# Optimization experiments

Hardware: AMD Instinct MI355X
Metric: run time of the kernel (lower is better)

Reference implementation:

```python
import jax, jax.numpy as jnp
import numpy as np

N, E, F_IN, HD, H, G, NG, OUT = 50000, 800000, 128, 64, 4, 512, 50, 64
HC = HD * H  # 256
LN_EPS = 1e-5

def _lin(k, fi, fo):
    return jax.random.normal(k, (fi, fo), jnp.float32) / np.sqrt(fi).astype(np.float32)

def setup_inputs() -> dict:
    key = jax.random.key(0)
    ks = jax.random.split(key, 26)
    x = jax.random.normal(ks[0], (N, F_IN), jnp.float32)
    edge_index = jax.random.randint(ks[1], (2, E), 0, N)
    batch = jnp.sort(jax.random.randint(ks[2], (N,), 0, G))
    group_ids = jax.random.randint(ks[3], (N,), 0, NG)
    inp = {
        'x': x, 'edge_index': edge_index, 'batch': batch, 'group_ids': group_ids,
        'group_table': jax.random.normal(ks[4], (NG, HD), jnp.float32),
        'inW': _lin(ks[5], F_IN + HD, HD), 'inb': jnp.zeros((HD,), jnp.float32),
        'inln_g': jnp.ones((HD,), jnp.float32), 'inln_b': jnp.zeros((HD,), jnp.float32),
        'W0': _lin(ks[6], HD, HC), 'as0': jax.random.normal(ks[7], (H, HD), jnp.float32) * 0.1,
        'ad0': jax.random.normal(ks[8], (H, HD), jnp.float32) * 0.1, 'b0': jnp.zeros((HC,), jnp.float32),
        'ln0g': jnp.ones((HC,), jnp.float32), 'ln0b': jnp.zeros((HC,), jnp.float32),
        'W1': _lin(ks[9], HC, HC), 'as1': jax.random.normal(ks[10], (H, HD), jnp.float32) * 0.1,
        'ad1': jax.random.normal(ks[11], (H, HD), jnp.float32) * 0.1, 'b1': jnp.zeros((HC,), jnp.float32),
        'ln1g': jnp.ones((HC,), jnp.float32), 'ln1b': jnp.zeros((HC,), jnp.float32),
        'fc1W': _lin(ks[12], HC, HD), 'fc1b': jnp.zeros((HD,), jnp.float32),
        'fc2W': _lin(ks[13], HD, OUT), 'fc2b': jnp.zeros((OUT,), jnp.float32),
    }
    return inp

def _layer_norm(x, g, b):
    mu = jnp.mean(x, axis=-1, keepdims=True)
    var = jnp.mean(jnp.square(x - mu), axis=-1, keepdims=True)
    return (x - mu) * jax.lax.rsqrt(var + LN_EPS) * g + b

def _gat_conv(x, src, dst, W, a_src, a_dst, bias):
    # x: [N, Fin] -> per-head projection [N, H, HD]
    xl = (x @ W).reshape(-1, H, HD)
    al_s = jnp.einsum('nhc,hc->nh', xl, a_src)  # [N, H]
    al_d = jnp.einsum('nhc,hc->nh', xl, a_dst)
    e = jax.nn.leaky_relu(al_s[src] + al_d[dst], 0.2)  # [Etot, H]
    m = jax.ops.segment_max(e, dst, num_segments=N)    # stable softmax over in-edges
    ex = jnp.exp(e - m[dst])
    s = jax.ops.segment_sum(ex, dst, num_segments=N)
    alpha = ex / (s[dst] + 1e-16)
    msg = xl[src] * alpha[:, :, None]                   # [Etot, H, HD]
    out = jax.ops.segment_sum(msg, dst, num_segments=N)
    return out.reshape(-1, HC) + bias

def reference(x, edge_index, batch, group_ids, group_table, inW, inb, inln_g, inln_b,
              W0, as0, ad0, b0, ln0g, ln0b, W1, as1, ad1, b1, ln1g, ln1b,
              fc1W, fc1b, fc2W, fc2b):
    # group embedding concat + input projection (Linear -> LN -> GELU)
    h = jnp.concatenate([x, group_table[group_ids]], axis=-1)
    h = jax.nn.gelu(_layer_norm(h @ inW + inb, inln_g, inln_b), approximate=False)
    # add self-loops (PyG GATConv default)
    loop = jnp.arange(N)
    src = jnp.concatenate([edge_index[0], loop])
    dst = jnp.concatenate([edge_index[1], loop])
    # layer 0: dims 64 -> 256, no residual (width mismatch)
    h = jax.nn.gelu(_layer_norm(_gat_conv(h, src, dst, W0, as0, ad0, b0), ln0g, ln0b), approximate=False)
    # layer 1: 256 -> 256, residual applies
    identity = h
    h = jax.nn.gelu(_layer_norm(_gat_conv(h, src, dst, W1, as1, ad1, b1), ln1g, ln1b), approximate=False)
    h = h + identity
    # global mean pool over graphs
    sums = jax.ops.segment_sum(h, batch, num_segments=G)
    cnt = jax.ops.segment_sum(jnp.ones((N, 1), h.dtype), batch, num_segments=G)
    pooled = sums / jnp.maximum(cnt, 1.0)
    z = jax.nn.gelu(pooled @ fc1W + fc1b, approximate=False)
    logits = z @ fc2W + fc2b
    return jax.nn.log_softmax(logits, axis=1)
```

## Files before the change

kernel.cpp:

```cpp
#include <hip/hip_runtime.h>
#include <math.h>

#define N_NODES 50000
#define N_EDGES 800000
#define ETOT (N_EDGES + N_NODES)
#define F_IN 128
#define HD 64
#define NHEAD 4
#define HC 256
#define NGRAPH 512
#define NOUT 64
#define LN_EPS 1e-5f

typedef __attribute__((ext_vector_type(8))) short bf16x8;
typedef __attribute__((ext_vector_type(4))) float f32x4;
typedef __attribute__((ext_vector_type(2))) float f32x2;

__device__ __forceinline__ float wave_sum(float v) {
#pragma unroll
    for (int m = 1; m < 64; m <<= 1) v += __shfl_xor(v, m, 64);
    return v;
}
__device__ __forceinline__ float wave_max(float v) {
#pragma unroll
    for (int m = 1; m < 64; m <<= 1) v = fmaxf(v, __shfl_xor(v, m, 64));
    return v;
}
__device__ __forceinline__ float red16(float v) {
    v += __shfl_xor(v, 1, 64);
    v += __shfl_xor(v, 2, 64);
    v += __shfl_xor(v, 4, 64);
    v += __shfl_xor(v, 8, 64);
    return v;
}
__device__ __forceinline__ float gelu_exact(float x) {
    return 0.5f * x * (1.0f + erff(x * 0.70710678118654752f));
}
__device__ __forceinline__ unsigned short f2bf(float x) {
    unsigned int u = __float_as_uint(x);
    return (unsigned short)((u + 0x7fffu + ((u >> 16) & 1u)) >> 16);
}
__device__ __forceinline__ float bf2f(unsigned short u) {
    return __uint_as_float(((unsigned int)u) << 16);
}

__global__ void k_count(const int* __restrict__ ei, int* __restrict__ deg) {
    int t = blockIdx.x * blockDim.x + threadIdx.x;
    if (t >= ETOT) return;
    int dst = (t < N_EDGES) ? ei[N_EDGES + t] : (t - N_EDGES);
    atomicAdd(deg + dst, 1);
}

__global__ void k_scan(const int* __restrict__ deg, int* __restrict__ rowptr,
                       int* __restrict__ cursor) {
    __shared__ int wsum[16];
    __shared__ int chunk_total;
    int tid = threadIdx.x, wid = tid >> 6, lane = tid & 63;
    int carry = 0;
    if (tid == 0) rowptr[0] = 0;
    for (int base = 0; base < N_NODES; base += 1024) {
        int i = base + tid;
        int v = (i < N_NODES) ? deg[i] : 0;
        int incl = v;
#pragma unroll
        for (int off = 1; off < 64; off <<= 1) {
            int t = __shfl_up(incl, off, 64);
            if (lane >= off) incl += t;
        }
        if (lane == 63) wsum[wid] = incl;
        __syncthreads();
        if (wid == 0) {
            int wv = (lane < 16) ? wsum[lane] : 0;
            int wincl = wv;
#pragma unroll
            for (int off = 1; off < 16; off <<= 1) {
                int t = __shfl_up(wincl, off, 64);
                if (lane >= off) wincl += t;
            }
            if (lane < 16) wsum[lane] = wincl - wv;
            if (lane == 15) chunk_total = wincl;
        }
        __syncthreads();
        int total_incl = carry + wsum[wid] + incl;
        if (i < N_NODES) {
            rowptr[i + 1] = total_incl;
            cursor[i] = total_incl - v;
        }
        carry += chunk_total;
        __syncthreads();
    }
}

__global__ void k_fill(const int* __restrict__ ei, int* __restrict__ cursor,
                       int* __restrict__ csr) {
    int t = blockIdx.x * blockDim.x + threadIdx.x;
    if (t >= ETOT) return;
    int src, dst;
    if (t < N_EDGES) { src = ei[t]; dst = ei[N_EDGES + t]; }
    else             { src = t - N_EDGES; dst = src; }
    int p = atomicAdd(cursor + dst, 1);
    csr[p] = src;
}

__global__ void k_pack_all(const float* __restrict__ inW, const float* __restrict__ W0,
                           const float* __restrict__ W1, const float* __restrict__ as0,
                           const float* __restrict__ ad0,
                           unsigned short* __restrict__ inWpk, unsigned short* __restrict__ W0pk,
                           unsigned short* __restrict__ W1pk, float* __restrict__ us,
                           float* __restrict__ ud) {
    int b = blockIdx.x;
    if (b < 48) {
        int tid = b * 256 + threadIdx.x;
        int i = tid & 7, l = (tid >> 3) & 63, t2 = tid >> 9;
        int nb = t2 % 4, kt = t2 / 4;
        int k = kt * 32 + ((l >> 4) << 3) + i;
        int n = nb * 16 + (l & 15);
        inWpk[tid] = f2bf(inW[k * 64 + n]);
    } else if (b < 112) {
        int tid = (b - 48) * 256 + threadIdx.x;
        int i = tid & 7, l = (tid >> 3) & 63, t2 = tid >> 9;
        int nb = t2 % 16, kt = t2 / 16;
        int q = kt * 32 + ((l >> 4) << 3) + i;
        int k = 16 * (q & 3) + (q >> 2);
        int n = nb * 16 + (l & 15);
        W0pk[tid] = f2bf(W0[k * 256 + n]);
    } else if (b < 368) {
        int tid = (b - 112) * 256 + threadIdx.x;
        int i = tid & 7, l = (tid >> 3) & 63, t2 = tid >> 9;
        int nb = t2 % 16, kt = t2 / 16;
        int k = kt * 32 + ((l >> 4) << 3) + i;
        int n = nb * 16 + (l & 15);
        W1pk[tid] = f2bf(W1[k * 256 + n]);
    } else {
        int t = threadIdx.x;
        int h = t >> 6, k2 = t & 63;
        float ss = 0.f, dd = 0.f;
        for (int c = 0; c < 64; c++) {
            float w = W0[k2 * 256 + h * 64 + c];
            ss += w * as0[h * 64 + c];
            dd += w * ad0[h * 64 + c];
        }
        us[t] = ss;
        ud[t] = dd;
    }
}

__global__ void k_proj_in_mma(const float* __restrict__ x, const int* __restrict__ gid,
                              const float* __restrict__ gt,
                              const unsigned short* __restrict__ Wpk,
                              const float* __restrict__ inb, const float* __restrict__ lng,
                              const float* __restrict__ lnb, const float* __restrict__ us,
                              const float* __restrict__ ud, unsigned int* __restrict__ h08,
                              float* __restrict__ als0, float* __restrict__ ald0) {
    int wid = threadIdx.x >> 6, lane = threadIdx.x & 63;
    int m0 = blockIdx.x * 64 + wid * 16;
    if (m0 >= N_NODES) return;
    int g16 = lane >> 4, c16 = lane & 15;
    int row_a = m0 + c16;
    int g = gid[row_a];
    f32x4 acc[4] = {{0,0,0,0},{0,0,0,0},{0,0,0,0},{0,0,0,0}};
#pragma unroll
    for (int kt = 0; kt < 6; kt++) {
        const float* src = (kt < 4) ? (x + (size_t)row_a * F_IN + kt * 32 + g16 * 8)
                                    : (gt + (size_t)g * HD + (kt - 4) * 32 + g16 * 8);
        float4 f0 = *(const float4*)(src);
        float4 f1 = *(const float4*)(src + 4);
        bf16x8 a;
        a[0] = (short)f2bf(f0.x); a[1] = (short)f2bf(f0.y);
        a[2] = (short)f2bf(f0.z); a[3] = (short)f2bf(f0.w);
        a[4] = (short)f2bf(f1.x); a[5] = (short)f2bf(f1.y);
        a[6] = (short)f2bf(f1.z); a[7] = (short)f2bf(f1.w);
#pragma unroll
        for (int nt = 0; nt < 4; nt++) {
            bf16x8 b = *(const bf16x8*)(Wpk + (((kt * 4 + nt) * 64 + lane) << 3));
            acc[nt] = __builtin_amdgcn_mfma_f32_16x16x32_bf16(a, b, acc[nt], 0, 0, 0);
        }
    }
    float bv[4], gv[4], bb[4];
    float usl[4][4], udl[4][4];
#pragma unroll
    for (int nt = 0; nt < 4; nt++) {
        int c = nt * 16 + c16;
        bv[nt] = inb[c]; gv[nt] = lng[c]; bb[nt] = lnb[c];
#pragma unroll
        for (int h = 0; h < 4; h++) {
            usl[h][nt] = us[h * 64 + c];
            udl[h][nt] = ud[h * 64 + c];
        }
    }
#pragma unroll
    for (int j = 0; j < 4; j++) {
        float d[4], s = 0.f;
#pragma unroll
        for (int nt = 0; nt < 4; nt++) { d[nt] = acc[nt][j] + bv[nt]; s += d[nt]; }
        float mu = red16(s) * (1.0f / 64.0f);
        float v = 0.f;
#pragma unroll
        for (int nt = 0; nt < 4; nt++) { d[nt] -= mu; v += d[nt] * d[nt]; }
        float r = rsqrtf(red16(v) * (1.0f / 64.0f) + LN_EPS);
        int row = m0 + g16 * 4 + j;
        float y0 = gelu_exact(d[0] * r * gv[0] + bb[0]);
        float y1 = gelu_exact(d[1] * r * gv[1] + bb[1]);
        float y2 = gelu_exact(d[2] * r * gv[2] + bb[2]);
        float y3 = gelu_exact(d[3] * r * gv[3] + bb[3]);
        int u = __builtin_amdgcn_cvt_pk_fp8_f32(y0, y1, 0, false);
        u = __builtin_amdgcn_cvt_pk_fp8_f32(y2, y3, u, true);
        h08[(size_t)row * 16 + c16] = (unsigned int)u;
        float ps0 = y0 * usl[0][0] + y1 * usl[0][1] + y2 * usl[0][2] + y3 * usl[0][3];
        float ps1 = y0 * usl[1][0] + y1 * usl[1][1] + y2 * usl[1][2] + y3 * usl[1][3];
        float ps2 = y0 * usl[2][0] + y1 * usl[2][1] + y2 * usl[2][2] + y3 * usl[2][3];
        float ps3 = y0 * usl[3][0] + y1 * usl[3][1] + y2 * usl[3][2] + y3 * usl[3][3];
        float pd0 = y0 * udl[0][0] + y1 * udl[0][1] + y2 * udl[0][2] + y3 * udl[0][3];
        float pd1 = y0 * udl[1][0] + y1 * udl[1][1] + y2 * udl[1][2] + y3 * udl[1][3];
        float pd2 = y0 * udl[2][0] + y1 * udl[2][1] + y2 * udl[2][2] + y3 * udl[2][3];
        float pd3 = y0 * udl[3][0] + y1 * udl[3][1] + y2 * udl[3][2] + y3 * udl[3][3];
        ps0 = red16(ps0); ps1 = red16(ps1); ps2 = red16(ps2); ps3 = red16(ps3);
        pd0 = red16(pd0); pd1 = red16(pd1); pd2 = red16(pd2); pd3 = red16(pd3);
        if (c16 == 0) {
            float4 s4 = {ps0, ps1, ps2, ps3};
            float4 d4 = {pd0, pd1, pd2, pd3};
            ((float4*)als0)[row] = s4;
            ((float4*)ald0)[row] = d4;
        }
    }
}

__global__ void k_agg0(const int* __restrict__ rowptr, const int* __restrict__ csr,
                       const unsigned int* __restrict__ h08, const float* __restrict__ als,
                       const float* __restrict__ ald, unsigned short* __restrict__ aggbf) {
    __shared__ float4 lacc[2][64];
    __shared__ float lss[2][4];
    int wid = threadIdx.x >> 6, lane = threadIdx.x & 63;
    int nloc = wid >> 1, half = wid & 1;
    int node = blockIdx.x * 2 + nloc;
    int start = rowptr[node], end = rowptr[node + 1];
    int g = lane >> 4, l16 = lane & 15;
    float4 adv = ((const float4*)ald)[node];
    int cntE = end - start;
    int mid = start + ((cntE + 1) >> 1);
    int k0 = half ? mid : start;
    int k1 = half ? end : mid;
    float a00 = 0, a01 = 0, a02 = 0, a03 = 0;
    float a10 = 0, a11 = 0, a12 = 0, a13 = 0;
    float a20 = 0, a21 = 0, a22 = 0, a23 = 0;
    float a30 = 0, a31 = 0, a32 = 0, a33 = 0;
    float s0 = 0, s1 = 0, s2 = 0, s3 = 0;
    const float4* als4 = (const float4*)als;
    for (int kb = k0; kb < k1; kb += 8) {
        int eA = kb + g, eB = kb + 4 + g;
        int cA = (eA < k1) ? eA : (k1 - 1);
        int cB = (eB < k1) ? eB : (k1 - 1);
        int snA = csr[cA], snB = csr[cB];
        float4 avA = als4[snA], avB = als4[snB];
        unsigned int uA = h08[(size_t)snA * 16 + l16];
        unsigned int uB = h08[(size_t)snB * 16 + l16];
        float eA0 = avA.x + adv.x; eA0 = fmaxf(eA0, 0.2f * eA0);
        float eA1 = avA.y + adv.y; eA1 = fmaxf(eA1, 0.2f * eA1);
        float eA2 = avA.z + adv.z; eA2 = fmaxf(eA2, 0.2f * eA2);
        float eA3 = avA.w + adv.w; eA3 = fmaxf(eA3, 0.2f * eA3);
        float wA0 = __expf(eA0), wA1 = __expf(eA1), wA2 = __expf(eA2), wA3 = __expf(eA3);
        if (eA >= k1) { wA0 = 0.f; wA1 = 0.f; wA2 = 0.f; wA3 = 0.f; }
        f32x2 loA = __builtin_amdgcn_cvt_pk_f32_fp8((int)uA, false);
        f32x2 hiA = __builtin_amdgcn_cvt_pk_f32_fp8((int)uA, true);
        s0 += wA0; s1 += wA1; s2 += wA2; s3 += wA3;
        float x0 = loA.x, x1 = loA.y, x2 = hiA.x, x3 = hiA.y;
        a00 += wA0 * x0; a01 += wA0 * x1; a02 += wA0 * x2; a03 += wA0 * x3;
        a10 += wA1 * x0; a11 += wA1 * x1; a12 += wA1 * x2; a13 += wA1 * x3;
        a20 += wA2 * x0; a21 += wA2 * x1; a22 += wA2 * x2; a23 += wA2 * x3;
        a30 += wA3 * x0; a31 += wA3 * x1; a32 += wA3 * x2; a33 += wA3 * x3;
        float eB0 = avB.x + adv.x; eB0 = fmaxf(eB0, 0.2f * eB0);
        float eB1 = avB.y + adv.y; eB1 = fmaxf(eB1, 0.2f * eB1);
        float eB2 = avB.z + adv.z; eB2 = fmaxf(eB2, 0.2f * eB2);
        float eB3 = avB.w + adv.w; eB3 = fmaxf(eB3, 0.2f * eB3);
        float wB0 = __expf(eB0), wB1 = __expf(eB1), wB2 = __expf(eB2), wB3 = __expf(eB3);
        if (eB >= k1) { wB0 = 0.f; wB1 = 0.f; wB2 = 0.f; wB3 = 0.f; }
        f32x2 loB = __builtin_amdgcn_cvt_pk_f32_fp8((int)uB, false);
        f32x2 hiB = __builtin_amdgcn_cvt_pk_f32_fp8((int)uB, true);
        s0 += wB0; s1 += wB1; s2 += wB2; s3 += wB3;
        float z0 = loB.x, z1 = loB.y, z2 = hiB.x, z3 = hiB.y;
        a00 += wB0 * z0; a01 += wB0 * z1; a02 += wB0 * z2; a03 += wB0 * z3;
        a10 += wB1 * z0; a11 += wB1 * z1; a12 += wB1 * z2; a13 += wB1 * z3;
        a20 += wB2 * z0; a21 += wB2 * z1; a22 += wB2 * z2; a23 += wB2 * z3;
        a30 += wB3 * z0; a31 += wB3 * z1; a32 += wB3 * z2; a33 += wB3 * z3;
    }
#define RED2(v) v += __shfl_xor(v, 16, 64); v += __shfl_xor(v, 32, 64)
    RED2(a00); RED2(a01); RED2(a02); RED2(a03);
    RED2(a10); RED2(a11); RED2(a12); RED2(a13);
    RED2(a20); RED2(a21); RED2(a22); RED2(a23);
    RED2(a30); RED2(a31); RED2(a32); RED2(a33);
    RED2(s0);  RED2(s1);  RED2(s2);  RED2(s3);
#undef RED2
    if (half) {
        float o0 = (g == 0) ? a00 : (g == 1) ? a10 : (g == 2) ? a20 : a30;
        float o1 = (g == 0) ? a01 : (g == 1) ? a11 : (g == 2) ? a21 : a31;
        float o2 = (g == 0) ? a02 : (g == 1) ? a12 : (g == 2) ? a22 : a32;
        float o3 = (g == 0) ? a03 : (g == 1) ? a13 : (g == 2) ? a23 : a33;
        float4 o = {o0, o1, o2, o3};
        lacc[nloc][lane] = o;
        if (lane < 4) {
            float sv = (lane == 0) ? s0 : (lane == 1) ? s1 : (lane == 2) ? s2 : s3;
            lss[nloc][lane] = sv;
        }
    }
    __syncthreads();
    if (!half) {
        float4 p0 = lacc[nloc][0 + l16];
        float4 p1 = lacc[nloc][16 + l16];
        float4 p2 = lacc[nloc][32 + l16];
        float4 p3 = lacc[nloc][48 + l16];
        a00 += p0.x; a01 += p0.y; a02 += p0.z; a03 += p0.w;
        a10 += p1.x; a11 += p1.y; a12 += p1.z; a13 += p1.w;
        a20 += p2.x; a21 += p2.y; a22 += p2.z; a23 += p2.w;
        a30 += p3.x; a31 += p3.y; a32 += p3.z; a33 += p3.w;
        s0 += lss[nloc][0]; s1 += lss[nloc][1];
        s2 += lss[nloc][2]; s3 += lss[nloc][3];
        float o0 = (g == 0) ? a00 : (g == 1) ? a10 : (g == 2) ? a20 : a30;
        float o1 = (g == 0) ? a01 : (g == 1) ? a11 : (g == 2) ? a21 : a31;
        float o2 = (g == 0) ? a02 : (g == 1) ? a12 : (g == 2) ? a22 : a32;
        float o3 = (g == 0) ? a03 : (g == 1) ? a13 : (g == 2) ? a23 : a33;
        float sg = (g == 0) ? s0 : (g == 1) ? s1 : (g == 2) ? s2 : s3;
        float inv = 1.0f / (sg + 1e-16f);
        ushort4 o = {f2bf(o0 * inv), f2bf(o1 * inv), f2bf(o2 * inv), f2bf(o3 * inv)};
        ((ushort4*)aggbf)[(size_t)node * 64 + lane] = o;
    }
}

__global__ void k_postgemm0(const unsigned short* __restrict__ A,
                            const unsigned short* __restrict__ Wpk,
                            const float* __restrict__ bias, const float* __restrict__ lng,
                            const float* __restrict__ lnb, unsigned short* __restrict__ h1bf) {
    int wid = threadIdx.x >> 6, lane = threadIdx.x & 63;
    int m0 = blockIdx.x * 64 + wid * 16;
    if (m0 >= N_NODES) return;
    int g16 = lane >> 4, c16 = lane & 15;
    f32x4 acc[16] = {};
#pragma unroll
    for (int h = 0; h < 4; h++) {
#pragma unroll
        for (int kt = 0; kt < 2; kt++) {
            bf16x8 a = *(const bf16x8*)(A + (size_t)(m0 + c16) * 256 + h * 64 + kt * 32 + g16 * 8);
#pragma unroll
            for (int nt = 0; nt < 4; nt++) {
                bf16x8 b = *(const bf16x8*)(Wpk + (((kt * 16 + h * 4 + nt) * 64 + lane) << 3));
                acc[h * 4 + nt] = __builtin_amdgcn_mfma_f32_16x16x32_bf16(a, b, acc[h * 4 + nt], 0, 0, 0);
            }
        }
    }
    float bv[16], gv[16], bb[16];
#pragma unroll
    for (int q = 0; q < 16; q++) {
        int c = q * 16 + c16;
        bv[q] = bias[c]; gv[q] = lng[c]; bb[q] = lnb[c];
    }
#pragma unroll
    for (int j = 0; j < 4; j++) {
        float d[16], ssum = 0.f;
#pragma unroll
        for (int q = 0; q < 16; q++) { d[q] = acc[q][j] + bv[q]; ssum += d[q]; }
        float mu = red16(ssum) * (1.0f / 256.0f);
        float v = 0.f;
#pragma unroll
        for (int q = 0; q < 16; q++) { d[q] -= mu; v += d[q] * d[q]; }
        float r = rsqrtf(red16(v) * (1.0f / 256.0f) + LN_EPS);
        int row = m0 + g16 * 4 + j;
#pragma unroll
        for (int q = 0; q < 16; q++) {
            float y = gelu_exact(d[q] * r * gv[q] + bb[q]);
            h1bf[(size_t)row * 256 + q * 16 + c16] = f2bf(y);
        }
    }
}

__global__ void k_proj_mma(const unsigned short* __restrict__ A,
                           const unsigned short* __restrict__ Wpk,
                           const float* __restrict__ as_, const float* __restrict__ ad_,
                           unsigned int* __restrict__ xl8, float* __restrict__ als,
                           float* __restrict__ ald) {
    int wid = threadIdx.x >> 6, lane = threadIdx.x & 63;
    int m0 = blockIdx.x * 16;
    int g16 = lane >> 4, c16 = lane & 15;
    f32x4 acc[4] = {{0,0,0,0},{0,0,0,0},{0,0,0,0},{0,0,0,0}};
#pragma unroll
    for (int kt = 0; kt < 8; kt++) {
        bf16x8 a = *(const bf16x8*)(A + (size_t)(m0 + c16) * 256 + kt * 32 + g16 * 8);
#pragma unroll
        for (int nt = 0; nt < 4; nt++) {
            bf16x8 b = *(const bf16x8*)(Wpk + (((kt * 16 + wid * 4 + nt) * 64 + lane) << 3));
            acc[nt] = __builtin_amdgcn_mfma_f32_16x16x32_bf16(a, b, acc[nt], 0, 0, 0);
        }
    }
    float asv[4], adv[4];
#pragma unroll
    for (int nt = 0; nt < 4; nt++) {
        int c = wid * 64 + nt * 16 + c16;
        asv[nt] = as_[c]; adv[nt] = ad_[c];
    }
#pragma unroll
    for (int j = 0; j < 4; j++) {
        int row = m0 + g16 * 4 + j;
        float v0 = acc[0][j], v1 = acc[1][j], v2 = acc[2][j], v3 = acc[3][j];
        int u = __builtin_amdgcn_cvt_pk_fp8_f32(v0, v1, 0, false);
        u = __builtin_amdgcn_cvt_pk_fp8_f32(v2, v3, u, true);
        xl8[(size_t)row * 64 + wid * 16 + c16] = (unsigned int)u;
        float ps = v0 * asv[0] + v1 * asv[1] + v2 * asv[2] + v3 * asv[3];
        float pd = v0 * adv[0] + v1 * adv[1] + v2 * adv[2] + v3 * adv[3];
        ps = red16(ps); pd = red16(pd);
        if (c16 == 0) { als[row * 4 + wid] = ps; ald[row * 4 + wid] = pd; }
    }
}

__global__ void k_agg1(const int* __restrict__ rowptr, const int* __restrict__ csr,
                       const unsigned int* __restrict__ xl8, const float* __restrict__ als,
                       const float* __restrict__ ald, const float* __restrict__ bias,
                       const float* __restrict__ lng, const float* __restrict__ lnb,
                       const unsigned short* __restrict__ identity_bf,
                       const int* __restrict__ batch, float* __restrict__ pooled,
                       int* __restrict__ cnt) {
    __shared__ float4 lacc[2][3][64];
    __shared__ float lss[2][3][64];
    __shared__ float4 lyout[2][64];
    __shared__ int lbatch[2];
    int wid = threadIdx.x >> 6, lane = threadIdx.x & 63;
    int nloc = wid >> 2, q = wid & 3;
    int node = blockIdx.x * 2 + nloc;
    int start = rowptr[node], end = rowptr[node + 1];
    int len = end - start;
    int head = lane >> 4, c16 = lane & 15;
    int fb = head * 64 + c16;
    float adh = ald[node * 4 + head];
    int k0 = start + (len * q) / 4;
    int k1 = start + (len * (q + 1)) / 4;
    float4 acc = {0.f, 0.f, 0.f, 0.f};
    float s = 0.f;
    int k = k0;
    for (; k + 4 <= k1; k += 4) {
        int sn0 = csr[k], sn1 = csr[k + 1], sn2 = csr[k + 2], sn3 = csr[k + 3];
        float e0 = als[sn0 * 4 + head] + adh;
        float e1 = als[sn1 * 4 + head] + adh;
        float e2 = als[sn2 * 4 + head] + adh;
        float e3 = als[sn3 * 4 + head] + adh;
        unsigned int u0 = xl8[(size_t)sn0 * 64 + lane];
        unsigned int u1 = xl8[(size_t)sn1 * 64 + lane];
        unsigned int u2 = xl8[(size_t)sn2 * 64 + lane];
        unsigned int u3 = xl8[(size_t)sn3 * 64 + lane];
        e0 = fmaxf(e0, 0.2f * e0); e1 = fmaxf(e1, 0.2f * e1);
        e2 = fmaxf(e2, 0.2f * e2); e3 = fmaxf(e3, 0.2f * e3);
        float a0 = __expf(e0), a1 = __expf(e1), a2 = __expf(e2), a3 = __expf(e3);
        s += a0 + a1 + a2 + a3;
        f32x2 lo0 = __builtin_amdgcn_cvt_pk_f32_fp8((int)u0, false);
        f32x2 hi0 = __builtin_amdgcn_cvt_pk_f32_fp8((int)u0, true);
        f32x2 lo1 = __builtin_amdgcn_cvt_pk_f32_fp8((int)u1, false);
        f32x2 hi1 = __builtin_amdgcn_cvt_pk_f32_fp8((int)u1, true);
        f32x2 lo2 = __builtin_amdgcn_cvt_pk_f32_fp8((int)u2, false);
        f32x2 hi2 = __builtin_amdgcn_cvt_pk_f32_fp8((int)u2, true);
        f32x2 lo3 = __builtin_amdgcn_cvt_pk_f32_fp8((int)u3, false);
        f32x2 hi3 = __builtin_amdgcn_cvt_pk_f32_fp8((int)u3, true);
        acc.x += a0 * lo0.x + a1 * lo1.x + a2 * lo2.x + a3 * lo3.x;
        acc.y += a0 * lo0.y + a1 * lo1.y + a2 * lo2.y + a3 * lo3.y;
        acc.z += a0 * hi0.x + a1 * hi1.x + a2 * hi2.x + a3 * hi3.x;
        acc.w += a0 * hi0.y + a1 * hi1.y + a2 * hi2.y + a3 * hi3.y;
    }
    for (; k < k1; k++) {
        int sn = csr[k];
        float e = als[sn * 4 + head] + adh;
        e = fmaxf(e, 0.2f * e);
        float a = __expf(e);
        s += a;
        unsigned int u = xl8[(size_t)sn * 64 + lane];
        f32x2 lo = __builtin_amdgcn_cvt_pk_f32_fp8((int)u, false);
        f32x2 hi = __builtin_amdgcn_cvt_pk_f32_fp8((int)u, true);
        acc.x += a * lo.x; acc.y += a * lo.y;
        acc.z += a * hi.x; acc.w += a * hi.y;
    }
    if (q) { lacc[nloc][q - 1][lane] = acc; lss[nloc][q - 1][lane] = s; }
    __syncthreads();
    if (q == 0) {
        float4 p0 = lacc[nloc][0][lane];
        float4 p1 = lacc[nloc][1][lane];
        float4 p2 = lacc[nloc][2][lane];
        acc.x += p0.x + p1.x + p2.x;
        acc.y += p0.y + p1.y + p2.y;
        acc.z += p0.z + p1.z + p2.z;
        acc.w += p0.w + p1.w + p2.w;
        s += lss[nloc][0][lane] + lss[nloc][1][lane] + lss[nloc][2][lane];
        float inv = 1.0f / (s + 1e-16f);
        acc.x = acc.x * inv + bias[fb];
        acc.y = acc.y * inv + bias[fb + 16];
        acc.z = acc.z * inv + bias[fb + 32];
        acc.w = acc.w * inv + bias[fb + 48];
        float mu = wave_sum(acc.x + acc.y + acc.z + acc.w) * (1.0f / 256.0f);
        float dx = acc.x - mu, dy = acc.y - mu, dz = acc.z - mu, dw = acc.w - mu;
        float var = wave_sum(dx * dx + dy * dy + dz * dz + dw * dw) * (1.0f / 256.0f);
        float r = rsqrtf(var + LN_EPS);
        float g0v = lng[fb], g1v = lng[fb + 16], g2v = lng[fb + 32], g3v = lng[fb + 48];
        float b0v = lnb[fb], b1v = lnb[fb + 16], b2v = lnb[fb + 32], b3v = lnb[fb + 48];
        const unsigned short* idp = identity_bf + (size_t)node * 256 + fb;
        float4 y;
        y.x = gelu_exact(dx * r * g0v + b0v) + bf2f(idp[0]);
        y.y = gelu_exact(dy * r * g1v + b1v) + bf2f(idp[16]);
        y.z = gelu_exact(dz * r * g2v + b2v) + bf2f(idp[32]);
        y.w = gelu_exact(dw * r * g3v + b3v) + bf2f(idp[48]);
        lyout[nloc][lane] = y;
        if (lane == 0) lbatch[nloc] = batch[node];
    }
    __syncthreads();
    if (wid == 0) {
        int g0 = lbatch[0], g1 = lbatch[1];
        float4 a = lyout[0][lane], b = lyout[1][lane];
        float* p0 = pooled + (size_t)g0 * 256 + fb;
        if (g0 == g1) {
            atomicAdd(p0 +  0, a.x + b.x); atomicAdd(p0 + 16, a.y + b.y);
            atomicAdd(p0 + 32, a.z + b.z); atomicAdd(p0 + 48, a.w + b.w);
            if (lane == 0) atomicAdd(cnt + g0, 2);
        } else {
            float* p1 = pooled + (size_t)g1 * 256 + fb;
            atomicAdd(p0 +  0, a.x); atomicAdd(p0 + 16, a.y);
            atomicAdd(p0 + 32, a.z); atomicAdd(p0 + 48, a.w);
            atomicAdd(p1 +  0, b.x); atomicAdd(p1 + 16, b.y);
            atomicAdd(p1 + 32, b.z); atomicAdd(p1 + 48, b.w);
            if (lane == 0) { atomicAdd(cnt + g0, 1); atomicAdd(cnt + g1, 1); }
        }
    }
}

__global__ void k_final(const float* __restrict__ pooled, const int* __restrict__ cnt,
                        const float* __restrict__ fc1W, const float* __restrict__ fc1b,
                        const float* __restrict__ fc2W, const float* __restrict__ fc2b,
                        float* __restrict__ out) {
    __shared__ float prow[4][256];
    __shared__ float zrow[4][64];
    int wid = threadIdx.x >> 6, lane = threadIdx.x & 63;
    int g = blockIdx.x * 4 + wid;
    float inv = 1.0f / fmaxf((float)cnt[g], 1.0f);
#pragma unroll
    for (int k = lane; k < 256; k += 64) prow[wid][k] = pooled[g * 256 + k] * inv;
    __syncthreads();
    float acc = fc1b[lane];
#pragma unroll 4
    for (int k = 0; k < 256; k++) acc += prow[wid][k] * fc1W[k * 64 + lane];
    zrow[wid][lane] = gelu_exact(acc);
    __syncthreads();
    float logit = fc2b[lane];
#pragma unroll 4
    for (int k = 0; k < 64; k++) logit += zrow[wid][k] * fc2W[k * 64 + lane];
    float mx = wave_max(logit);
    float se = wave_sum(__expf(logit - mx));
    out[g * NOUT + lane] = logit - mx - logf(se);
}

extern "C" void kernel_launch(void* const* d_in, const int* in_sizes, int n_in,
                              void* d_out, int out_size, void* d_ws, size_t ws_size,
                              hipStream_t stream) {
    const float* x     = (const float*)d_in[0];
    const int*   ei    = (const int*)d_in[1];
    const int*   batch = (const int*)d_in[2];
    const int*   gid   = (const int*)d_in[3];
    const float* gt    = (const float*)d_in[4];
    const float* inW   = (const float*)d_in[5];
    const float* inb   = (const float*)d_in[6];
    const float* inlng = (const float*)d_in[7];
    const float* inlnb = (const float*)d_in[8];
    const float* W0    = (const float*)d_in[9];
    const float* as0   = (const float*)d_in[10];
    const float* ad0   = (const float*)d_in[11];
    const float* b0    = (const float*)d_in[12];
    const float* ln0g  = (const float*)d_in[13];
    const float* ln0b  = (const float*)d_in[14];
    const float* W1    = (const float*)d_in[15];
    const float* as1   = (const float*)d_in[16];
    const float* ad1   = (const float*)d_in[17];
    const float* b1    = (const float*)d_in[18];
    const float* ln1g  = (const float*)d_in[19];
    const float* ln1b  = (const float*)d_in[20];
    const float* fc1W  = (const float*)d_in[21];
    const float* fc1b  = (const float*)d_in[22];
    const float* fc2W  = (const float*)d_in[23];
    const float* fc2b  = (const float*)d_in[24];
    float* out = (float*)d_out;

    char* ws = (char*)d_ws;
    size_t off = 0;
    auto alloc = [&](size_t bytes) {
        void* p = ws + off;
        off += (bytes + 255) / 256 * 256;
        return p;
    };
    unsigned int*   h08    = (unsigned int*)alloc((size_t)N_NODES * 16 * 4);
    unsigned short* agg0bf = (unsigned short*)alloc((size_t)N_NODES * 256 * 2);
    unsigned short* h1bf   = (unsigned short*)alloc((size_t)N_NODES * 256 * 2);
    unsigned int*   xl8    = (unsigned int*)alloc((size_t)N_NODES * 64 * 4);
    unsigned short* inWpk  = (unsigned short*)alloc((size_t)192 * 64 * 2);
    unsigned short* W0pk   = (unsigned short*)alloc((size_t)64 * 256 * 2);
    unsigned short* W1pk   = (unsigned short*)alloc((size_t)256 * 256 * 2);
    float* us     = (float*)alloc((size_t)256 * 4);
    float* ud     = (float*)alloc((size_t)256 * 4);
    float* als0   = (float*)alloc((size_t)N_NODES * 4 * 4);
    float* ald0   = (float*)alloc((size_t)N_NODES * 4 * 4);
    float* als1   = (float*)alloc((size_t)N_NODES * 4 * 4);
    float* ald1   = (float*)alloc((size_t)N_NODES * 4 * 4);
    int*   rowptr = (int*)alloc((size_t)(N_NODES + 1) * 4);
    int*   cursor = (int*)alloc((size_t)N_NODES * 4);
    int*   csr    = (int*)alloc((size_t)ETOT * 4);
    float* pooled = (float*)alloc((size_t)NGRAPH * 256 * 4);
    int*   cnt    = (int*)alloc((size_t)NGRAPH * 4);
    int*   deg    = (int*)alloc((size_t)N_NODES * 4);
    size_t zspan = ((char*)deg + (size_t)N_NODES * 4) - (char*)pooled;

    hipMemsetAsync(pooled, 0, zspan, stream);

    int eb = (ETOT + 255) / 256;
    k_count<<<eb, 256, 0, stream>>>(ei, deg);
    k_scan<<<1, 1024, 0, stream>>>(deg, rowptr, cursor);
    k_fill<<<eb, 256, 0, stream>>>(ei, cursor, csr);

    k_pack_all<<<369, 256, 0, stream>>>(inW, W0, W1, as0, ad0, inWpk, W0pk, W1pk, us, ud);

    k_proj_in_mma<<<(N_NODES + 63) / 64, 256, 0, stream>>>(x, gid, gt, inWpk, inb, inlng, inlnb,
                                                           us, ud, h08, als0, ald0);
    k_agg0<<<N_NODES / 2, 256, 0, stream>>>(rowptr, csr, h08, als0, ald0, agg0bf);
    k_postgemm0<<<(N_NODES + 63) / 64, 256, 0, stream>>>(agg0bf, W0pk, b0, ln0g, ln0b, h1bf);
    k_proj_mma<<<N_NODES / 16, 256, 0, stream>>>(h1bf, W1pk, as1, ad1, xl8, als1, ald1);
    k_agg1<<<N_NODES / 2, 512, 0, stream>>>(rowptr, csr, xl8, als1, ald1, b1, ln1g, ln1b,
                                            h1bf, batch, pooled, cnt);
    k_final<<<NGRAPH / 4, 256, 0, stream>>>(pooled, cnt, fc1W, fc1b, fc2W, fc2b, out);
}
```

Measured before the change: 435.6 us.

## Merge degree count into pack kernel, simplify scan, halve agg1 edge split

Degree counting now runs as extra blocks of the weight-packing kernel, which removes one launch and lets the two independent jobs overlap. The single-block scan now gives each thread a contiguous chunk of 49 nodes and does one block-wide scan, replacing the serial loop over 1024-node chunks with its repeated barriers. k_agg1 now splits each node's in-edges across 2 waves instead of 4 (256 threads per block), which cuts shared-memory reduction work but leaves less parallelism per node for high-degree nodes.

```diff
diff --git a/kernel.cpp b/kernel.cpp
--- a/kernel.cpp
+++ b/kernel.cpp
@@ -4,6 +4,7 @@
 #define N_NODES 50000
 #define N_EDGES 800000
 #define ETOT (N_EDGES + N_NODES)
+#define EB ((ETOT + 255) / 256)
 #define F_IN 128
 #define HD 64
 #define NHEAD 4
@@ -44,71 +45,22 @@
     return __uint_as_float(((unsigned int)u) << 16);
 }
 
-__global__ void k_count(const int* __restrict__ ei, int* __restrict__ deg) {
-    int t = blockIdx.x * blockDim.x + threadIdx.x;
-    if (t >= ETOT) return;
-    int dst = (t < N_EDGES) ? ei[N_EDGES + t] : (t - N_EDGES);
-    atomicAdd(deg + dst, 1);
-}
-
-__global__ void k_scan(const int* __restrict__ deg, int* __restrict__ rowptr,
-                       int* __restrict__ cursor) {
-    __shared__ int wsum[16];
-    __shared__ int chunk_total;
-    int tid = threadIdx.x, wid = tid >> 6, lane = tid & 63;
-    int carry = 0;
-    if (tid == 0) rowptr[0] = 0;
-    for (int base = 0; base < N_NODES; base += 1024) {
-        int i = base + tid;
-        int v = (i < N_NODES) ? deg[i] : 0;
-        int incl = v;
-#pragma unroll
-        for (int off = 1; off < 64; off <<= 1) {
-            int t = __shfl_up(incl, off, 64);
-            if (lane >= off) incl += t;
-        }
-        if (lane == 63) wsum[wid] = incl;
-        __syncthreads();
-        if (wid == 0) {
-            int wv = (lane < 16) ? wsum[lane] : 0;
-            int wincl = wv;
-#pragma unroll
-            for (int off = 1; off < 16; off <<= 1) {
-                int t = __shfl_up(wincl, off, 64);
-                if (lane >= off) wincl += t;
-            }
-            if (lane < 16) wsum[lane] = wincl - wv;
-            if (lane == 15) chunk_total = wincl;
-        }
-        __syncthreads();
-        int total_incl = carry + wsum[wid] + incl;
-        if (i < N_NODES) {
-            rowptr[i + 1] = total_incl;
-            cursor[i] = total_incl - v;
-        }
-        carry += chunk_total;
-        __syncthreads();
-    }
-}
-
-__global__ void k_fill(const int* __restrict__ ei, int* __restrict__ cursor,
-                       int* __restrict__ csr) {
-    int t = blockIdx.x * blockDim.x + threadIdx.x;
-    if (t >= ETOT) return;
-    int src, dst;
-    if (t < N_EDGES) { src = ei[t]; dst = ei[N_EDGES + t]; }
-    else             { src = t - N_EDGES; dst = src; }
-    int p = atomicAdd(cursor + dst, 1);
-    csr[p] = src;
-}
-
-__global__ void k_pack_all(const float* __restrict__ inW, const float* __restrict__ W0,
-                           const float* __restrict__ W1, const float* __restrict__ as0,
-                           const float* __restrict__ ad0,
+__global__ void k_prep_all(const int* __restrict__ ei, const float* __restrict__ inW,
+                           const float* __restrict__ W0, const float* __restrict__ W1,
+                           const float* __restrict__ as0, const float* __restrict__ ad0,
+                           int* __restrict__ deg,
                            unsigned short* __restrict__ inWpk, unsigned short* __restrict__ W0pk,
                            unsigned short* __restrict__ W1pk, float* __restrict__ us,
                            float* __restrict__ ud) {
     int b = blockIdx.x;
+    if (b < EB) {
+        int t = b * 256 + threadIdx.x;
+        if (t >= ETOT) return;
+        int dst = (t < N_EDGES) ? ei[N_EDGES + t] : (t - N_EDGES);
+        atomicAdd(deg + dst, 1);
+        return;
+    }
+    b -= EB;
     if (b < 48) {
         int tid = b * 256 + threadIdx.x;
         int i = tid & 7, l = (tid >> 3) & 63, t2 = tid >> 9;
@@ -143,6 +95,62 @@
         us[t] = ss;
         ud[t] = dd;
     }
+}
+
+__global__ void k_scan(const int* __restrict__ deg, int* __restrict__ rowptr,
+                       int* __restrict__ cursor) {
+    const int PER = 49;
+    __shared__ int wsum[16];
+    int tid = threadIdx.x, wid = tid >> 6, lane = tid & 63;
+    int base = tid * PER;
+    int sum = 0;
+#pragma unroll 7
+    for (int i = 0; i < PER; i++) {
+        int idx = base + i;
+        if (idx < N_NODES) sum += deg[idx];
+    }
+    int incl = sum;
+#pragma unroll
+    for (int off = 1; off < 64; off <<= 1) {
+        int t = __shfl_up(incl, off, 64);
+        if (lane >= off) incl += t;
+    }
+    if (lane == 63) wsum[wid] = incl;
+    __syncthreads();
+    if (wid == 0) {
+        int wv = (lane < 16) ? wsum[lane] : 0;
+        int wincl = wv;
+#pragma unroll
+        for (int off = 1; off < 16; off <<= 1) {
+            int t = __shfl_up(wincl, off, 64);
+            if (lane >= off) wincl += t;
+        }
+        if (lane < 16) wsum[lane] = wincl - wv;
+    }
+    __syncthreads();
+    int run = wsum[wid] + incl - sum;
+    if (tid == 0) rowptr[0] = 0;
+#pragma unroll 7
+    for (int i = 0; i < PER; i++) {
+        int idx = base + i;
+        if (idx < N_NODES) {
+            int v = deg[idx];
+            cursor[idx] = run;
+            run += v;
+            rowptr[idx + 1] = run;
+        }
+    }
+}
+
+__global__ void k_fill(const int* __restrict__ ei, int* __restrict__ cursor,
+                       int* __restrict__ csr) {
+    int t = blockIdx.x * blockDim.x + threadIdx.x;
+    if (t >= ETOT) return;
+    int src, dst;
+    if (t < N_EDGES) { src = ei[t]; dst = ei[N_EDGES + t]; }
+    else             { src = t - N_EDGES; dst = src; }
+    int p = atomicAdd(cursor + dst, 1);
+    csr[p] = src;
 }
 
 __global__ void k_proj_in_mma(const float* __restrict__ x, const int* __restrict__ gid,
@@ -416,20 +424,21 @@
                        const unsigned short* __restrict__ identity_bf,
                        const int* __restrict__ batch, float* __restrict__ pooled,
                        int* __restrict__ cnt) {
-    __shared__ float4 lacc[2][3][64];
-    __shared__ float lss[2][3][64];
+    __shared__ float4 lacc[2][64];
+    __shared__ float lss[2][64];
     __shared__ float4 lyout[2][64];
     __shared__ int lbatch[2];
     int wid = threadIdx.x >> 6, lane = threadIdx.x & 63;
-    int nloc = wid >> 2, q = wid & 3;
+    int nloc = wid >> 1, half = wid & 1;
     int node = blockIdx.x * 2 + nloc;
     int start = rowptr[node], end = rowptr[node + 1];
-    int len = end - start;
     int head = lane >> 4, c16 = lane & 15;
     int fb = head * 64 + c16;
     float adh = ald[node * 4 + head];
-    int k0 = start + (len * q) / 4;
-    int k1 = start + (len * (q + 1)) / 4;
+    int cntE = end - start;
+    int mid = start + ((cntE + 1) >> 1);
+    int k0 = half ? mid : start;
+    int k1 = half ? end : mid;
     float4 acc = {0.f, 0.f, 0.f, 0.f};
     float s = 0.f;
     int k = k0;
@@ -472,17 +481,12 @@
         acc.x += a * lo.x; acc.y += a * lo.y;
         acc.z += a * hi.x; acc.w += a * hi.y;
     }
-    if (q) { lacc[nloc][q - 1][lane] = acc; lss[nloc][q - 1][lane] = s; }
+    if (half) { lacc[nloc][lane] = acc; lss[nloc][lane] = s; }
     __syncthreads();
-    if (q == 0) {
-        float4 p0 = lacc[nloc][0][lane];
-        float4 p1 = lacc[nloc][1][lane];
-        float4 p2 = lacc[nloc][2][lane];
-        acc.x += p0.x + p1.x + p2.x;
-        acc.y += p0.y + p1.y + p2.y;
-        acc.z += p0.z + p1.z + p2.z;
-        acc.w += p0.w + p1.w + p2.w;
-        s += lss[nloc][0][lane] + lss[nloc][1][lane] + lss[nloc][2][lane];
+    if (!half) {
+        float4 p = lacc[nloc][lane];
+        acc.x += p.x; acc.y += p.y; acc.z += p.z; acc.w += p.w;
+        s += lss[nloc][lane];
         float inv = 1.0f / (s + 1e-16f);
         acc.x = acc.x * inv + bias[fb];
         acc.y = acc.y * inv + bias[fb + 16];
@@ -608,19 +612,17 @@
 
     hipMemsetAsync(pooled, 0, zspan, stream);
 
-    int eb = (ETOT + 255) / 256;
-    k_count<<<eb, 256, 0, stream>>>(ei, deg);
+    k_prep_all<<<EB + 369, 256, 0, stream>>>(ei, inW, W0, W1, as0, ad0, deg,
+                                             inWpk, W0pk, W1pk, us, ud);
     k_scan<<<1, 1024, 0, stream>>>(deg, rowptr, cursor);
-    k_fill<<<eb, 256, 0, stream>>>(ei, cursor, csr);
-
-    k_pack_all<<<369, 256, 0, stream>>>(inW, W0, W1, as0, ad0, inWpk, W0pk, W1pk, us, ud);
+    k_fill<<<EB, 256, 0, stream>>>(ei, cursor, csr);
 
     k_proj_in_mma<<<(N_NODES + 63) / 64, 256, 0, stream>>>(x, gid, gt, inWpk, inb, inlng, inlnb,
                                                            us, ud, h08, als0, ald0);
     k_agg0<<<N_NODES / 2, 256, 0, stream>>>(rowptr, csr, h08, als0, ald0, agg0bf);
     k_postgemm0<<<(N_NODES + 63) / 64, 256, 0, stream>>>(agg0bf, W0pk, b0, ln0g, ln0b, h1bf);
     k_proj_mma<<<N_NODES / 16, 256, 0, stream>>>(h1bf, W1pk, as1, ad1, xl8, als1, ald1);
-    k_agg1<<<N_NODES / 2, 512, 0, stream>>>(rowptr, csr, xl8, als1, ald1, b1, ln1g, ln1b,
+    k_agg1<<<N_NODES / 2, 256, 0, stream>>>(rowptr, csr, xl8, als1, ald1, b1, ln1g, ln1b,
                                             h1bf, batch, pooled, cnt);
     k_final<<<NGRAPH / 4, 256, 0, stream>>>(pooled, cnt, fc1W, fc1b, fc2W, fc2b, out);
 }
```

Measured after the change: 473.2 us. 8.6% more time.
